# Performance work log

Measured on AMD Instinct MI355X. Metric: run time of the kernel, lower is better.

Reference implementation:

```python
import jax, jax.numpy as jnp
import numpy as np

# pywt db2 decomposition filters (len 4)
_DEC_LO = np.array([-0.12940952255126037, 0.22414386804201339, 0.8365163037378079, 0.48296291314453416], dtype=np.float32)
_DEC_HI = np.array([-0.48296291314453416, 0.8365163037378079, -0.22414386804201339, -0.12940952255126037], dtype=np.float32)


def _dwt1d(x, filt, axis):
    # pywt-style single-level DWT along `axis`, mode='symmetric'.
    x = jnp.moveaxis(x, axis, -1)
    L = x.shape[-1]
    flen = filt.shape[0]
    pad = [(0, 0)] * (x.ndim - 1) + [(flen - 1, flen - 1)]
    ext = jnp.pad(x, pad, mode='symmetric')            # (..., L + 2*flen - 2)
    outlen = (L + flen - 1) // 2
    fr = filt[::-1]
    out = None
    for k in range(flen):  # tiny fixed loop over 4 taps
        tap = jax.lax.slice_in_dim(ext, 1 + k, 1 + k + 2 * outlen, 2, axis=-1)
        out = fr[k] * tap if out is None else out + fr[k] * tap
    return jnp.moveaxis(out, -1, axis)


def _dwt2(x):
    lo = jnp.asarray(_DEC_LO)
    hi = jnp.asarray(_DEC_HI)
    lo_w = _dwt1d(x, lo, -1)
    cA = _dwt1d(lo_w, lo, -2)   # approx-approx
    cH = _dwt1d(lo_w, hi, -2)   # detail along H, approx along W (pywt cH)
    return cA, cH


def setup_inputs() -> dict:
    key = jax.random.key(0)
    ks = jax.random.split(key, 4)
    B, C, H, W = 8, 128, 256, 256
    hidden = C // 11  # reduction = 11
    x = jax.random.normal(ks[0], (B, C, H, W), dtype=jnp.float32)
    w1 = jax.random.normal(ks[1], (C, hidden), dtype=jnp.float32) * 0.05
    b1 = jnp.zeros((hidden,), dtype=jnp.float32)
    w2 = jax.random.normal(ks[2], (hidden, C), dtype=jnp.float32) * 0.05
    b2 = jnp.zeros((C,), dtype=jnp.float32)
    w_sa = jax.random.normal(ks[3], (1, 2, 5, 5), dtype=jnp.float32) * 0.05
    return {"x": x, "w1": w1, "b1": b1, "w2": w2, "b2": b2, "w_sa": w_sa}


def reference(x, w1, b1, w2, b2, w_sa):
    B, C, H, W = x.shape
    cA, cH = _dwt2(x)                                   # [B,C,Hc,Wc]
    # channel attention: avg-pool(cA) + max-pool(cH) -> MLP -> sigmoid
    avg_pool = jnp.mean(cA, axis=(2, 3))                # [B,C]
    max_pool = jnp.max(cH, axis=(2, 3))                 # [B,C]
    p = avg_pool + max_pool
    h = jax.nn.relu(p @ w1 + b1)
    channel_att = jax.nn.sigmoid(h @ w2 + b2)           # [B,C]
    channel_att = channel_att[:, :, None, None]
    # spatial attention on concat(cA, cH) over channels
    sp = jnp.concatenate([cA, cH], axis=1)              # [B,2C,Hc,Wc]
    avg_out = jnp.mean(sp, axis=1, keepdims=True)
    max_out = jnp.max(sp, axis=1, keepdims=True)
    sa_in = jnp.concatenate([avg_out, max_out], axis=1) # [B,2,Hc,Wc]
    sa = jax.lax.conv_general_dilated(
        sa_in, w_sa, window_strides=(1, 1), padding=[(2, 2), (2, 2)],
        dimension_numbers=("NCHW", "OIHW", "NCHW"))     # [B,1,Hc,Wc]
    sa = jax.nn.sigmoid(sa)
    # upsample the half-resolution spatial map back to (H, W) to gate x
    sa = jax.image.resize(sa, (B, 1, H, W), method="bilinear")
    return x * channel_att * sa
```

## Files before the change

kernel.cpp:

```cpp
#include <hip/hip_runtime.h>
#include <math.h>

#define B_N 8
#define C_CH 128
#define H_IN 256
#define W_IN 256
#define HO 129
#define WO 129
#define SP (HO*WO)
#define HIDDEN 11
#define NSTR 16
#define SH 8
#define NGE 32
#define CPW 4
#define WOP 132

__constant__ float c_lo[4] = {-0.12940952255126037f, 0.2241438680420134f,
                               0.8365163037378079f,  0.48296291314453416f};
__constant__ float c_hi[4] = {-0.48296291314453416f, 0.8365163037378079f,
                              -0.2241438680420134f, -0.12940952255126037f};

__global__ __launch_bounds__(256, 4) void dwt_stream_kernel(
    const float* __restrict__ x,
    float* __restrict__ psum, float* __restrict__ pmax,
    float* __restrict__ chpsum, float* __restrict__ chpmax)
{
  const int bid  = blockIdx.x;
  const int s    = bid & (NSTR - 1);
  const int gb   = (bid >> 4) & 7;
  const int b    = bid >> 7;
  const int tid  = threadIdx.x;
  const int lane = tid & 63;
  const int wave = tid >> 6;
  const int g    = gb * 4 + wave;
  const int cb   = g * CPW;
  const int j0   = s * SH;

  const float* xb = x + ((size_t)(b * C_CH + cb)) * (H_IN * W_IN) + 4 * lane;

  float W0[CPW][3], W1[CPW][3], W2[CPW][3], W3[CPW][3];
  #pragma unroll
  for (int ch = 0; ch < CPW; ++ch)
    #pragma unroll
    for (int sl = 0; sl < 3; ++sl) {
      W0[ch][sl] = 0.f; W1[ch][sl] = 0.f; W2[ch][sl] = 0.f; W3[ch][sl] = 0.f;
    }

  float sA[CPW], mH[CPW];
  #pragma unroll
  for (int ch = 0; ch < CPW; ++ch) { sA[ch] = 0.f; mH[ch] = -INFINITY; }

  const float l03 = c_lo[0] + c_lo[3], l12 = c_lo[1] + c_lo[2];
  const float h03 = c_hi[0] + c_hi[3], h12 = c_hi[1] + c_hi[2];

  float* cps = chpsum + ((size_t)(b * NGE + g)) * (HO * WOP);
  float* cpm = chpmax + ((size_t)(b * NGE + g)) * (HO * WOP);

  auto row_step = [&](int r) {
    #pragma unroll
    for (int ch = 0; ch < CPW; ++ch) {
      float4 v = *reinterpret_cast<const float4*>(xb + ch * (H_IN * W_IN) + r * W_IN);
      float pz = __shfl_up(v.z, 1);
      float pw = __shfl_up(v.w, 1);
      float l0 = (lane == 0)
                   ? (l03 * v.y + l12 * v.x)
                   : (c_lo[0]*v.y + c_lo[1]*v.x + c_lo[2]*pw + c_lo[3]*pz);
      float l1 = c_lo[0]*v.w + c_lo[1]*v.z + c_lo[2]*v.y + c_lo[3]*v.x;
      float l2 = l03 * v.z + l12 * v.w;
      W0[ch][0]=W1[ch][0]; W1[ch][0]=W2[ch][0]; W2[ch][0]=W3[ch][0]; W3[ch][0]=l0;
      W0[ch][1]=W1[ch][1]; W1[ch][1]=W2[ch][1]; W2[ch][1]=W3[ch][1]; W3[ch][1]=l1;
      W0[ch][2]=W1[ch][2]; W1[ch][2]=W2[ch][2]; W2[ch][2]=W3[ch][2]; W3[ch][2]=l2;
    }
  };

  auto store_cross = [&](int jo, float cs0, float cs1, float cs2,
                         float cm0, float cm1, float cm2) {
    float* ps = cps + (size_t)jo * WOP;
    float* pm = cpm + (size_t)jo * WOP;
    *reinterpret_cast<float2*>(ps + 2 * lane) = make_float2(cs0, cs1);
    *reinterpret_cast<float2*>(pm + 2 * lane) = make_float2(cm0, cm1);
    if (lane == 63) { ps[128] = cs2; pm[128] = cm2; }
  };

  auto emit_normal = [&](int jo) {
    float cs0=0.f, cs1=0.f, cs2=0.f, cm0=-INFINITY, cm1=-INFINITY, cm2=-INFINITY;
    #pragma unroll
    for (int ch = 0; ch < CPW; ++ch) {
      float a0 = c_lo[0]*W3[ch][0] + c_lo[1]*W2[ch][0] + c_lo[2]*W1[ch][0] + c_lo[3]*W0[ch][0];
      float h0 = c_hi[0]*W3[ch][0] + c_hi[1]*W2[ch][0] + c_hi[2]*W1[ch][0] + c_hi[3]*W0[ch][0];
      float a1 = c_lo[0]*W3[ch][1] + c_lo[1]*W2[ch][1] + c_lo[2]*W1[ch][1] + c_lo[3]*W0[ch][1];
      float h1 = c_hi[0]*W3[ch][1] + c_hi[1]*W2[ch][1] + c_hi[2]*W1[ch][1] + c_hi[3]*W0[ch][1];
      float a2 = c_lo[0]*W3[ch][2] + c_lo[1]*W2[ch][2] + c_lo[2]*W1[ch][2] + c_lo[3]*W0[ch][2];
      float h2 = c_hi[0]*W3[ch][2] + c_hi[1]*W2[ch][2] + c_hi[2]*W1[ch][2] + c_hi[3]*W0[ch][2];
      sA[ch] += a0 + a1;
      mH[ch] = fmaxf(mH[ch], fmaxf(h0, h1));
      if (lane == 63) { sA[ch] += a2; mH[ch] = fmaxf(mH[ch], h2); }
      cs0 += a0 + h0; cs1 += a1 + h1; cs2 += a2 + h2;
      cm0 = fmaxf(cm0, fmaxf(a0, h0));
      cm1 = fmaxf(cm1, fmaxf(a1, h1));
      cm2 = fmaxf(cm2, fmaxf(a2, h2));
    }
    store_cross(jo, cs0, cs1, cs2, cm0, cm1, cm2);
  };

  auto emit_top = [&]() {
    float cs0=0.f, cs1=0.f, cs2=0.f, cm0=-INFINITY, cm1=-INFINITY, cm2=-INFINITY;
    #pragma unroll
    for (int ch = 0; ch < CPW; ++ch) {
      float a0 = l03*W3[ch][0] + l12*W2[ch][0];
      float h0 = h03*W3[ch][0] + h12*W2[ch][0];
      float a1 = l03*W3[ch][1] + l12*W2[ch][1];
      float h1 = h03*W3[ch][1] + h12*W2[ch][1];
      float a2 = l03*W3[ch][2] + l12*W2[ch][2];
      float h2 = h03*W3[ch][2] + h12*W2[ch][2];
      sA[ch] += a0 + a1;
      mH[ch] = fmaxf(mH[ch], fmaxf(h0, h1));
      if (lane == 63) { sA[ch] += a2; mH[ch] = fmaxf(mH[ch], h2); }
      cs0 += a0 + h0; cs1 += a1 + h1; cs2 += a2 + h2;
      cm0 = fmaxf(cm0, fmaxf(a0, h0));
      cm1 = fmaxf(cm1, fmaxf(a1, h1));
      cm2 = fmaxf(cm2, fmaxf(a2, h2));
    }
    store_cross(0, cs0, cs1, cs2, cm0, cm1, cm2);
  };

  auto emit_bot = [&]() {
    float cs0=0.f, cs1=0.f, cs2=0.f, cm0=-INFINITY, cm1=-INFINITY, cm2=-INFINITY;
    #pragma unroll
    for (int ch = 0; ch < CPW; ++ch) {
      float a0 = l03*W2[ch][0] + l12*W3[ch][0];
      float h0 = h03*W2[ch][0] + h12*W3[ch][0];
      float a1 = l03*W2[ch][1] + l12*W3[ch][1];
      float h1 = h03*W2[ch][1] + h12*W3[ch][1];
      float a2 = l03*W2[ch][2] + l12*W3[ch][2];
      float h2 = h03*W2[ch][2] + h12*W3[ch][2];
      sA[ch] += a0 + a1;
      mH[ch] = fmaxf(mH[ch], fmaxf(h0, h1));
      if (lane == 63) { sA[ch] += a2; mH[ch] = fmaxf(mH[ch], h2); }
      cs0 += a0 + h0; cs1 += a1 + h1; cs2 += a2 + h2;
      cm0 = fmaxf(cm0, fmaxf(a0, h0));
      cm1 = fmaxf(cm1, fmaxf(a1, h1));
      cm2 = fmaxf(cm2, fmaxf(a2, h2));
    }
    store_cross(128, cs0, cs1, cs2, cm0, cm1, cm2);
  };

  if (s == 0) {
    row_step(0); row_step(1);
    emit_top();
    for (int k = 1; k < SH; ++k) {
      row_step(2*k); row_step(2*k + 1);
      emit_normal(k);
    }
  } else {
    row_step(2*j0 - 2); row_step(2*j0 - 1);
    for (int k = j0; k < j0 + SH; ++k) {
      row_step(2*k); row_step(2*k + 1);
      emit_normal(k);
    }
    if (s == NSTR - 1) emit_bot();
  }

  #pragma unroll
  for (int ch = 0; ch < CPW; ++ch) {
    float ssum = sA[ch], smax = mH[ch];
    for (int off = 32; off > 0; off >>= 1) {
      ssum += __shfl_down(ssum, off, 64);
      smax = fmaxf(smax, __shfl_down(smax, off, 64));
    }
    if (lane == 0) {
      size_t bc = (size_t)(b * C_CH + cb + ch);
      psum[bc * NSTR + s] = ssum;
      pmax[bc * NSTR + s] = smax;
    }
  }
}

__global__ __launch_bounds__(256) void combine_kernel(
    const float* __restrict__ chpsum, const float* __restrict__ chpmax,
    float* __restrict__ sa_in)
{
  int b = blockIdx.y;
  int s = blockIdx.x * 256 + threadIdx.x;
  if (s >= SP) return;
  int jo  = s / WO;
  int col = s - jo * WO;
  size_t off = (size_t)jo * WOP + col;
  float sum = 0.f, mx = -INFINITY;
  #pragma unroll 4
  for (int gg = 0; gg < NGE; ++gg) {
    sum += chpsum[((size_t)(b * NGE + gg)) * (HO * WOP) + off];
    mx = fmaxf(mx, chpmax[((size_t)(b * NGE + gg)) * (HO * WOP) + off]);
  }
  sa_in[(size_t)b * 2 * SP + s]      = sum * (1.f / 256.f);
  sa_in[(size_t)b * 2 * SP + SP + s] = mx;
}

__global__ __launch_bounds__(128) void mlp_kernel(
    const float* __restrict__ psum, const float* __restrict__ pmax,
    const float* __restrict__ w1, const float* __restrict__ b1,
    const float* __restrict__ w2, const float* __restrict__ b2,
    float* __restrict__ att)
{
  int b = blockIdx.x;
  int c = threadIdx.x;
  __shared__ float p[C_CH];
  __shared__ float h[HIDDEN];

  float s = 0.f, m = -INFINITY;
  #pragma unroll
  for (int k = 0; k < NSTR; ++k) {
    s += psum[(b * C_CH + c) * NSTR + k];
    m = fmaxf(m, pmax[(b * C_CH + c) * NSTR + k]);
  }
  p[c] = s * (1.f / 16641.f) + m;
  __syncthreads();

  if (c < HIDDEN) {
    float acc = b1[c];
    for (int k = 0; k < C_CH; ++k) acc += p[k] * w1[k * HIDDEN + c];
    h[c] = fmaxf(acc, 0.f);
  }
  __syncthreads();

  float acc = b2[c];
  #pragma unroll
  for (int j = 0; j < HIDDEN; ++j) acc += h[j] * w2[j * C_CH + c];
  att[b * C_CH + c] = 1.f / (1.f + expf(-acc));
}

__global__ __launch_bounds__(256) void conv_kernel(
    const float* __restrict__ sa_in, const float* __restrict__ w_sa,
    float* __restrict__ sa)
{
  int b = blockIdx.y;
  int s = blockIdx.x * 256 + threadIdx.x;
  if (s >= SP) return;
  int i = s / WO;
  int j = s - i * WO;
  float acc = 0.f;
  const float* in0 = sa_in + (size_t)b * 2 * SP;
  #pragma unroll
  for (int ch = 0; ch < 2; ++ch) {
    const float* in = in0 + ch * SP;
    #pragma unroll
    for (int u = 0; u < 5; ++u) {
      int ii = i + u - 2;
      if (ii < 0 || ii >= HO) continue;
      #pragma unroll
      for (int v = 0; v < 5; ++v) {
        int jj = j + v - 2;
        if (jj < 0 || jj >= WO) continue;
        acc += in[ii * WO + jj] * w_sa[(ch * 5 + u) * 5 + v];
      }
    }
  }
  sa[(size_t)b * SP + s] = 1.f / (1.f + expf(-acc));
}

__global__ __launch_bounds__(256) void resize_kernel(
    const float* __restrict__ sa, float* __restrict__ sar)
{
  int idx = blockIdx.x * 256 + threadIdx.x;
  int J = idx & 255;
  int I = (idx >> 8) & 255;
  int b = idx >> 16;

  float ti = (I + 0.5f) * (129.f / 256.f) - 0.5f;
  ti = fminf(fmaxf(ti, 0.f), 128.f);
  int i0 = (int)ti;
  float fi = ti - (float)i0;
  int i1 = min(i0 + 1, 128);

  float tj = (J + 0.5f) * (129.f / 256.f) - 0.5f;
  tj = fminf(fmaxf(tj, 0.f), 128.f);
  int jj0 = (int)tj;
  float fj = tj - (float)jj0;
  int jj1 = min(jj0 + 1, 128);

  const float* r0 = sa + ((size_t)b * HO + i0) * WO;
  const float* r1 = sa + ((size_t)b * HO + i1) * WO;
  float v0 = r0[jj0] + fj * (r0[jj1] - r0[jj0]);
  float v1 = r1[jj0] + fj * (r1[jj1] - r1[jj0]);
  sar[idx] = v0 + fi * (v1 - v0);
}

__global__ __launch_bounds__(256) void final2_kernel(
    const float* __restrict__ x, const float* __restrict__ att,
    const float* __restrict__ sar, float* __restrict__ out)
{
  int bid = blockIdx.x;
  int cchunk = bid & 3;
  int rg  = (bid >> 2) & 63;
  int b   = bid >> 8;
  int t = threadIdx.x;
  int r = t >> 6;
  int col4 = t & 63;
  int I = rg * 4 + r;

  __shared__ float att_s[32];
  if (t < 32) att_s[t] = att[b * C_CH + cchunk * 32 + t];
  __syncthreads();

  float4 sv = reinterpret_cast<const float4*>(sar + ((size_t)b * 256 + I) * 256)[col4];

  size_t base4 = ((size_t)(b * C_CH + cchunk * 32) * 256 + I) * 64 + col4;
  const float4* xp = reinterpret_cast<const float4*>(x);
  float4* op = reinterpret_cast<float4*>(out);
  #pragma unroll 4
  for (int cc = 0; cc < 32; ++cc) {
    float a = att_s[cc];
    float4 xv = xp[base4 + (size_t)cc * 16384];
    float4 ov;
    ov.x = xv.x * a * sv.x;
    ov.y = xv.y * a * sv.y;
    ov.z = xv.z * a * sv.z;
    ov.w = xv.w * a * sv.w;
    op[base4 + (size_t)cc * 16384] = ov;
  }
}

extern "C" void kernel_launch(void* const* d_in, const int* in_sizes, int n_in,
                              void* d_out, int out_size, void* d_ws, size_t ws_size,
                              hipStream_t stream) {
  const float* x    = (const float*)d_in[0];
  const float* w1   = (const float*)d_in[1];
  const float* b1   = (const float*)d_in[2];
  const float* w2   = (const float*)d_in[3];
  const float* b2   = (const float*)d_in[4];
  const float* w_sa = (const float*)d_in[5];
  float* out = (float*)d_out;

  float* chpsum = (float*)d_ws;
  float* chpmax = chpsum + (size_t)B_N * NGE * HO * WOP;
  float* psum   = chpmax + (size_t)B_N * NGE * HO * WOP;
  float* pmax   = psum + B_N * C_CH * NSTR;
  float* sa_in  = pmax + B_N * C_CH * NSTR;
  float* att    = sa_in + (size_t)B_N * 2 * SP;
  float* sa     = att + B_N * C_CH;
  float* sar    = sa + (size_t)B_N * SP;

  hipLaunchKernelGGL(dwt_stream_kernel, dim3(B_N * 8 * NSTR), dim3(256), 0, stream,
                     x, psum, pmax, chpsum, chpmax);
  hipLaunchKernelGGL(combine_kernel, dim3((SP + 255) / 256, B_N), dim3(256), 0, stream,
                     chpsum, chpmax, sa_in);
  hipLaunchKernelGGL(mlp_kernel, dim3(B_N), dim3(C_CH), 0, stream,
                     psum, pmax, w1, b1, w2, b2, att);
  hipLaunchKernelGGL(conv_kernel, dim3((SP + 255) / 256, B_N), dim3(256), 0, stream,
                     sa_in, w_sa, sa);
  hipLaunchKernelGGL(resize_kernel, dim3(B_N * H_IN * W_IN / 256), dim3(256), 0, stream,
                     sa, sar);
  hipLaunchKernelGGL(final2_kernel, dim3(B_N * 64 * 4), dim3(256), 0, stream,
                     x, att, sar, out);
}
```

Measured before the change: 218.7 us.

## Software-pipeline row-pair loads in DWT stream kernel with register double buffering

```diff
diff --git a/kernel.cpp b/kernel.cpp
--- a/kernel.cpp
+++ b/kernel.cpp
@@ -20,7 +20,7 @@
 __constant__ float c_hi[4] = {-0.48296291314453416f, 0.8365163037378079f,
                               -0.2241438680420134f, -0.12940952255126037f};
 
-__global__ __launch_bounds__(256, 4) void dwt_stream_kernel(
+__global__ __launch_bounds__(256) void dwt_stream_kernel(
     const float* __restrict__ x,
     float* __restrict__ psum, float* __restrict__ pmax,
     float* __restrict__ chpsum, float* __restrict__ chpmax)
@@ -56,21 +56,28 @@
   float* cps = chpsum + ((size_t)(b * NGE + g)) * (HO * WOP);
   float* cpm = chpmax + ((size_t)(b * NGE + g)) * (HO * WOP);
 
-  auto row_step = [&](int r) {
+  float4 cur0[CPW], cur1[CPW], nxt0[CPW], nxt1[CPW];
+
+  auto load_pair = [&](int r, float4* v0, float4* v1) {
     #pragma unroll
     for (int ch = 0; ch < CPW; ++ch) {
-      float4 v = *reinterpret_cast<const float4*>(xb + ch * (H_IN * W_IN) + r * W_IN);
-      float pz = __shfl_up(v.z, 1);
-      float pw = __shfl_up(v.w, 1);
-      float l0 = (lane == 0)
-                   ? (l03 * v.y + l12 * v.x)
-                   : (c_lo[0]*v.y + c_lo[1]*v.x + c_lo[2]*pw + c_lo[3]*pz);
-      float l1 = c_lo[0]*v.w + c_lo[1]*v.z + c_lo[2]*v.y + c_lo[3]*v.x;
-      float l2 = l03 * v.z + l12 * v.w;
-      W0[ch][0]=W1[ch][0]; W1[ch][0]=W2[ch][0]; W2[ch][0]=W3[ch][0]; W3[ch][0]=l0;
-      W0[ch][1]=W1[ch][1]; W1[ch][1]=W2[ch][1]; W2[ch][1]=W3[ch][1]; W3[ch][1]=l1;
-      W0[ch][2]=W1[ch][2]; W1[ch][2]=W2[ch][2]; W2[ch][2]=W3[ch][2]; W3[ch][2]=l2;
-    }
+      const float* p = xb + ch * (H_IN * W_IN) + r * W_IN;
+      v0[ch] = *reinterpret_cast<const float4*>(p);
+      v1[ch] = *reinterpret_cast<const float4*>(p + W_IN);
+    }
+  };
+
+  auto hrow = [&](float4 v, int ch) {
+    float pz = __shfl_up(v.z, 1);
+    float pw = __shfl_up(v.w, 1);
+    float l0 = (lane == 0)
+                 ? (l03 * v.y + l12 * v.x)
+                 : (c_lo[0]*v.y + c_lo[1]*v.x + c_lo[2]*pw + c_lo[3]*pz);
+    float l1 = c_lo[0]*v.w + c_lo[1]*v.z + c_lo[2]*v.y + c_lo[3]*v.x;
+    float l2 = l03 * v.z + l12 * v.w;
+    W0[ch][0]=W1[ch][0]; W1[ch][0]=W2[ch][0]; W2[ch][0]=W3[ch][0]; W3[ch][0]=l0;
+    W0[ch][1]=W1[ch][1]; W1[ch][1]=W2[ch][1]; W2[ch][1]=W3[ch][1]; W3[ch][1]=l1;
+    W0[ch][2]=W1[ch][2]; W1[ch][2]=W2[ch][2]; W2[ch][2]=W3[ch][2]; W3[ch][2]=l2;
   };
 
   auto store_cross = [&](int jo, float cs0, float cs1, float cs2,
@@ -145,21 +152,29 @@
     store_cross(128, cs0, cs1, cs2, cm0, cm1, cm2);
   };
 
-  if (s == 0) {
-    row_step(0); row_step(1);
-    emit_top();
-    for (int k = 1; k < SH; ++k) {
-      row_step(2*k); row_step(2*k + 1);
-      emit_normal(k);
-    }
-  } else {
-    row_step(2*j0 - 2); row_step(2*j0 - 1);
-    for (int k = j0; k < j0 + SH; ++k) {
-      row_step(2*k); row_step(2*k + 1);
-      emit_normal(k);
-    }
-    if (s == NSTR - 1) emit_bot();
-  }
+  const int rstart = (s == 0) ? 0 : (2 * j0 - 2);
+  const int npairs = (s == 0) ? SH : (SH + 1);
+
+  load_pair(rstart, cur0, cur1);
+  for (int p = 0; p < npairs; ++p) {
+    const bool last = (p + 1 == npairs);
+    if (!last) load_pair(rstart + 2 * (p + 1), nxt0, nxt1);
+
+    #pragma unroll
+    for (int ch = 0; ch < CPW; ++ch) { hrow(cur0[ch], ch); hrow(cur1[ch], ch); }
+
+    if (s == 0) {
+      if (p == 0) emit_top(); else emit_normal(p);
+    } else if (p > 0) {
+      emit_normal(j0 + p - 1);
+    }
+
+    if (!last) {
+      #pragma unroll
+      for (int ch = 0; ch < CPW; ++ch) { cur0[ch] = nxt0[ch]; cur1[ch] = nxt1[ch]; }
+    }
+  }
+  if (s == NSTR - 1) emit_bot();
 
   #pragma unroll
   for (int ch = 0; ch < CPW; ++ch) {
```

After: 210.6 us. 3.7% less time.
